# Optimization experiments

Measured on AMD Instinct MI355X. Metric: run time of the kernel, lower is better.

Reference implementation:

```python
import jax, jax.numpy as jnp
import numpy as np

B, N, S, K = 8, 16384, 1024, 32
C_STEM, C_PATCH, PE_DIM = 64, 128, 24
RADIUS = 0.2
NUM_BANDS = PE_DIM // 6  # 4 freq bands, sin+cos per xyz axis -> 3*2*4 = 24


def setup_inputs() -> dict:
    key = jax.random.key(0)
    ks = jax.random.split(key, 6)
    xyz = jax.random.uniform(ks[0], (B, N, 3), dtype=jnp.float32)
    point_feature = jax.random.normal(ks[1], (B, N, C_STEM), dtype=jnp.float32)
    patch_center = jax.random.uniform(ks[2], (B, S, 3), dtype=jnp.float32)
    in_dim = C_STEM + 3 + PE_DIM  # grouped_feature + relative_xyz + pos-enc
    w1 = jax.random.normal(ks[3], (in_dim, C_PATCH), dtype=jnp.float32) / np.sqrt(in_dim)
    b1 = jnp.zeros((C_PATCH,), dtype=jnp.float32)
    w2 = jax.random.normal(ks[4], (C_PATCH, C_PATCH), dtype=jnp.float32) / np.sqrt(C_PATCH)
    b2 = jnp.zeros((C_PATCH,), dtype=jnp.float32)
    return dict(xyz=xyz, point_feature=point_feature, patch_center=patch_center,
                w1=w1, b1=b1, w2=w2, b2=b2)


def query_ball_point(radius, nsample, xyz, new_xyz):
    # Standard PointNet++ ball query. xyz:[B,N,3], new_xyz:[B,S,3] -> idx:[B,S,K]
    n = xyz.shape[1]
    sqrdists = jnp.sum((new_xyz[:, :, None, :] - xyz[:, None, :, :]) ** 2, axis=-1)  # [B,S,N]
    gi = jnp.where(sqrdists > radius * radius, n,
                   jnp.arange(n, dtype=jnp.int32)[None, None, :])
    gi = jnp.sort(gi, axis=-1)[:, :, :nsample]           # first K in-ball indices
    first = gi[:, :, :1]
    gi = jnp.where(gi == n, first, gi)                   # pad misses with first hit
    return jnp.minimum(gi, n - 1)


def index_points(points, idx):
    # points:[B,N,C], idx:[B,S,K] -> [B,S,K,C]
    b = points.shape[0]
    return points[jnp.arange(b)[:, None, None], idx]


def pos_encode(rel):
    # NeRF-style sinusoidal encoding of relative xyz: [...,3] -> [...,PE_DIM]
    freqs = (2.0 ** jnp.arange(NUM_BANDS, dtype=jnp.float32)) * jnp.pi
    ang = rel[..., None] * freqs                          # [...,3,NB]
    enc = jnp.concatenate([jnp.sin(ang), jnp.cos(ang)], axis=-1)  # [...,3,2NB]
    return enc.reshape(rel.shape[:-1] + (PE_DIM,))


def reference(xyz, point_feature, patch_center, w1, b1, w2, b2):
    neighbor_idx = query_ball_point(RADIUS, K, xyz, patch_center)   # [B,S,K]
    grouped_xyz = index_points(xyz, neighbor_idx)                    # [B,S,K,3]
    grouped_feature = index_points(point_feature, neighbor_idx)      # [B,S,K,C_STEM]
    relative_xyz = grouped_xyz - patch_center[:, :, None, :]
    relative_position = pos_encode(relative_xyz)                     # [B,S,K,PE_DIM]
    grouped_input = jnp.concatenate(
        (grouped_feature, relative_xyz, relative_position), axis=-1)  # [B,S,K,91]
    h = jax.nn.relu(grouped_input @ w1 + b1)   # PointMLP 1 (shared per-point MLP)
    h = h @ w2 + b2                            # PointMLP 2 (no activation)
    patch_feature = jnp.max(h, axis=2)         # max-pool over K neighbors -> [B,S,C_PATCH]
    return (patch_feature, neighbor_idx)
```

## Files before the change

kernel.cpp:

```cpp
#include <hip/hip_runtime.h>
#include <hip/hip_bf16.h>

#define B_ 8
#define N_ 16384
#define S_ 1024
#define K_ 32
#define CSTEM 64
#define CPATCH 128
#define INDIM 91
#define LDA 104
#define LDH 136
#define NQ 4

typedef __attribute__((ext_vector_type(8))) short short8v;
typedef __attribute__((ext_vector_type(4))) float f32x4;

static __device__ __forceinline__ unsigned short f2bf(float f) {
  union { float f; unsigned int u; } v; v.f = f;
  return (unsigned short)((v.u + 0x7FFFu + ((v.u >> 16) & 1u)) >> 16);
}

__global__ __launch_bounds__(256) void pack_weights(
    const float* __restrict__ w1, const float* __restrict__ w2,
    unsigned short* __restrict__ w1p, unsigned short* __restrict__ w2p)
{
  const int id = blockIdx.x * 256 + threadIdx.x;
  if (id < 3 * 8 * 64) {
    const int l = id & 63, ct = (id >> 6) & 7, ks = id >> 9;
    const int col = 16 * ct + (l & 15);
    const int kb = 32 * ks + (l >> 4) * 8;
    unsigned short v[8];
    #pragma unroll
    for (int j = 0; j < 8; ++j) {
      const int k = kb + j;
      v[j] = (k < INDIM) ? f2bf(w1[k * CPATCH + col]) : (unsigned short)0;
    }
    *(short8v*)&w1p[(size_t)id * 8] = *(const short8v*)v;
  } else if (id < 3 * 8 * 64 + 4 * 8 * 64) {
    const int id2 = id - 3 * 8 * 64;
    const int l = id2 & 63, ct = (id2 >> 6) & 7, ks = id2 >> 9;
    const int col = 16 * ct + (l & 15);
    const int kb = 32 * ks + (l >> 4) * 8;
    unsigned short v[8];
    #pragma unroll
    for (int j = 0; j < 8; ++j) v[j] = f2bf(w2[(kb + j) * CPATCH + col]);
    *(short8v*)&w2p[(size_t)id2 * 8] = *(const short8v*)v;
  }
}

#define FCOMP(V, IDX) (((IDX) & 3) == 0 ? (V)[(IDX) >> 2].x : \
                       ((IDX) & 3) == 1 ? (V)[(IDX) >> 2].y : \
                       ((IDX) & 3) == 2 ? (V)[(IDX) >> 2].z : (V)[(IDX) >> 2].w)

__global__ __launch_bounds__(256) void fused_patch(
    const float* __restrict__ xyz, const float* __restrict__ pf,
    const float* __restrict__ pc,
    const unsigned short* __restrict__ w1p, const float* __restrict__ b1,
    const unsigned short* __restrict__ w2p, const float* __restrict__ b2,
    float* __restrict__ idx_out, float* __restrict__ out)
{
  const int tid  = threadIdx.x;
  const int lane = tid & 63;
  const int w    = tid >> 6;
  const int bs0  = blockIdx.x * NQ;
  const int b    = bs0 >> 10;

  __shared__ float scen[3 * NQ];
  __shared__ int   sidx[NQ][K_];
  __shared__ float sxyz[NQ][K_][3];
  __shared__ int   sfound[NQ];
  __shared__ __align__(16) unsigned short As[NQ * K_][LDA];
  __shared__ __align__(16) unsigned short Hs[K_][LDH];

  const float* __restrict__ xb  = xyz + (size_t)b * N_ * 3;
  const float* __restrict__ pfb = pf  + (size_t)b * N_ * CSTEM;

  if (tid < 3 * NQ) scen[tid] = pc[bs0 * 3 + tid];
  __syncthreads();

  {
    const int q = w;
    const float cx = scen[q * 3 + 0];
    const float cy = scen[q * 3 + 1];
    const float cz = scen[q * 3 + 2];
    const double rr = 0.2 * 0.2;

    int found = 0;
    for (int base = 0; base < N_; base += 1024) {
      const int i0 = base + lane * 16;
      float4 v[12];
      #pragma unroll
      for (int t = 0; t < 12; ++t)
        v[t] = *(const float4*)&xb[i0 * 3 + t * 4];

      unsigned mask = 0u;
      #pragma unroll
      for (int p = 0; p < 16; ++p) {
        const float X = FCOMP(v, 3 * p + 0);
        const float Y = FCOMP(v, 3 * p + 1);
        const float Z = FCOMP(v, 3 * p + 2);
        const float dxf = X - cx, dyf = Y - cy, dzf = Z - cz;
        const float d2f = fmaf(dxf, dxf, fmaf(dyf, dyf, dzf * dzf));
        bool in;
        if (fabsf(d2f - 0.04f) <= 1e-5f) {
          const double dx = (double)X - (double)cx;
          const double dy = (double)Y - (double)cy;
          const double dz = (double)Z - (double)cz;
          in = (dx * dx + dy * dy + dz * dz) <= rr;
        } else {
          in = (d2f < 0.04f);
        }
        if (in) mask |= (1u << p);
      }

      const int cnt = __popc(mask);
      int incl = cnt;
      #pragma unroll
      for (int d = 1; d < 64; d <<= 1) {
        const int t = __shfl_up(incl, d);
        if (lane >= d) incl += t;
      }
      const int tot = __shfl(incl, 63);

      int pos = found + (incl - cnt);
      #pragma unroll
      for (int p = 0; p < 16; ++p) {
        if (mask & (1u << p)) {
          if (pos < K_) {
            sidx[q][pos] = i0 + p;
            sxyz[q][pos][0] = FCOMP(v, 3 * p + 0);
            sxyz[q][pos][1] = FCOMP(v, 3 * p + 1);
            sxyz[q][pos][2] = FCOMP(v, 3 * p + 2);
          }
          ++pos;
        }
      }
      found += tot;
      if (found >= K_) break;
    }
    if (lane == 0) sfound[q] = found;
  }
  __syncthreads();

  if (tid < NQ && sfound[tid] == 0) {
    sidx[tid][0] = N_ - 1;
    sxyz[tid][0][0] = xb[(N_ - 1) * 3 + 0];
    sxyz[tid][0][1] = xb[(N_ - 1) * 3 + 1];
    sxyz[tid][0][2] = xb[(N_ - 1) * 3 + 2];
  }
  __syncthreads();
  if (tid < NQ * K_) {
    const int q = tid >> 5, j = tid & 31;
    const int fq = sfound[q];
    const int v   = (j < fq && fq > 0) ? sidx[q][j]    : sidx[q][0];
    const float x = (j < fq && fq > 0) ? sxyz[q][j][0] : sxyz[q][0][0];
    const float y = (j < fq && fq > 0) ? sxyz[q][j][1] : sxyz[q][0][1];
    const float z = (j < fq && fq > 0) ? sxyz[q][j][2] : sxyz[q][0][2];
    sidx[q][j] = v;
    sxyz[q][j][0] = x; sxyz[q][j][1] = y; sxyz[q][j][2] = z;
    idx_out[(size_t)bs0 * K_ + tid] = (float)v;
  }
  __syncthreads();

  short8v w1f[3][2], w2f[4][2];
  #pragma unroll
  for (int ks = 0; ks < 3; ++ks)
    #pragma unroll
    for (int t = 0; t < 2; ++t)
      w1f[ks][t] = *(const short8v*)&w1p[((size_t)(ks * 8 + 2 * w + t) * 64 + lane) * 8];
  #pragma unroll
  for (int ks = 0; ks < 4; ++ks)
    #pragma unroll
    for (int t = 0; t < 2; ++t)
      w2f[ks][t] = *(const short8v*)&w2p[((size_t)(ks * 8 + 2 * w + t) * 64 + lane) * 8];
  const float bias1[2] = { b1[32 * w + (lane & 15)], b1[32 * w + 16 + (lane & 15)] };
  const float bias2[2] = { b2[32 * w + (lane & 15)], b2[32 * w + 16 + (lane & 15)] };

  {
    const int row = tid >> 3, sub = tid & 7;
    #pragma unroll
    for (int q = 0; q < NQ; ++q) {
      const int r = sidx[q][row];
      const float4 f0 = *(const float4*)&pfb[(size_t)r * CSTEM + sub * 8];
      const float4 f1 = *(const float4*)&pfb[(size_t)r * CSTEM + sub * 8 + 4];
      unsigned short vv[8];
      vv[0] = f2bf(f0.x); vv[1] = f2bf(f0.y); vv[2] = f2bf(f0.z); vv[3] = f2bf(f0.w);
      vv[4] = f2bf(f1.x); vv[5] = f2bf(f1.y); vv[6] = f2bf(f1.z); vv[7] = f2bf(f1.w);
      *(short8v*)&As[q * K_ + row][sub * 8] = *(const short8v*)vv;
    }
  }
  {
    const int row = tid & 31, j = tid >> 5;
    #pragma unroll
    for (int q = 0; q < NQ; ++q) {
      const float r0 = sxyz[q][row][0] - scen[q * 3 + 0];
      const float r1 = sxyz[q][row][1] - scen[q * 3 + 1];
      const float r2 = sxyz[q][row][2] - scen[q * 3 + 2];
      #pragma unroll
      for (int cc = 0; cc < 4; ++cc) {
        const int c = 64 + 4 * j + cc;
        float val;
        if (c < 67) val = (c == 64) ? r0 : ((c == 65) ? r1 : r2);
        else if (c < 91) {
          const int qq = c - 67, d = qq >> 3, rbit = qq & 7, band = rbit & 3;
          const float rel = (d == 0) ? r0 : ((d == 1) ? r1 : r2);
          const float ang = rel * ((float)(1 << band) * 3.14159265358979323846f);
          val = (rbit < 4) ? __sinf(ang) : __cosf(ang);
        } else val = 0.f;
        As[q * K_ + row][c] = f2bf(val);
      }
    }
  }
  __syncthreads();

  #pragma unroll 1
  for (int q = 0; q < NQ; ++q) {
    f32x4 acc[2][2] = {};
    #pragma unroll
    for (int ks = 0; ks < 3; ++ks) {
      const int k0 = ks * 32 + (lane >> 4) * 8;
      const short8v a0 = *(const short8v*)&As[q * K_ + (lane & 15)][k0];
      const short8v a1 = *(const short8v*)&As[q * K_ + 16 + (lane & 15)][k0];
      acc[0][0] = __builtin_amdgcn_mfma_f32_16x16x32_bf16(a0, w1f[ks][0], acc[0][0], 0, 0, 0);
      acc[0][1] = __builtin_amdgcn_mfma_f32_16x16x32_bf16(a0, w1f[ks][1], acc[0][1], 0, 0, 0);
      acc[1][0] = __builtin_amdgcn_mfma_f32_16x16x32_bf16(a1, w1f[ks][0], acc[1][0], 0, 0, 0);
      acc[1][1] = __builtin_amdgcn_mfma_f32_16x16x32_bf16(a1, w1f[ks][1], acc[1][1], 0, 0, 0);
    }
    #pragma unroll
    for (int rt = 0; rt < 2; ++rt)
      #pragma unroll
      for (int t = 0; t < 2; ++t)
        #pragma unroll
        for (int reg = 0; reg < 4; ++reg) {
          const float h = fmaxf(acc[rt][t][reg] + bias1[t], 0.f);
          const int row = 16 * rt + (lane >> 4) * 4 + reg;
          const int col = 32 * w + 16 * t + (lane & 15);
          Hs[row][col] = f2bf(h);
        }
    __syncthreads();

    f32x4 acc2[2][2] = {};
    #pragma unroll
    for (int ks = 0; ks < 4; ++ks) {
      const int k0 = ks * 32 + (lane >> 4) * 8;
      const short8v a0 = *(const short8v*)&Hs[(lane & 15)][k0];
      const short8v a1 = *(const short8v*)&Hs[16 + (lane & 15)][k0];
      acc2[0][0] = __builtin_amdgcn_mfma_f32_16x16x32_bf16(a0, w2f[ks][0], acc2[0][0], 0, 0, 0);
      acc2[0][1] = __builtin_amdgcn_mfma_f32_16x16x32_bf16(a0, w2f[ks][1], acc2[0][1], 0, 0, 0);
      acc2[1][0] = __builtin_amdgcn_mfma_f32_16x16x32_bf16(a1, w2f[ks][0], acc2[1][0], 0, 0, 0);
      acc2[1][1] = __builtin_amdgcn_mfma_f32_16x16x32_bf16(a1, w2f[ks][1], acc2[1][1], 0, 0, 0);
    }
    float m0 = -3.4e38f, m1 = -3.4e38f;
    #pragma unroll
    for (int rt = 0; rt < 2; ++rt)
      #pragma unroll
      for (int reg = 0; reg < 4; ++reg) {
        m0 = fmaxf(m0, acc2[rt][0][reg]);
        m1 = fmaxf(m1, acc2[rt][1][reg]);
      }
    m0 += bias2[0];
    m1 += bias2[1];
    m0 = fmaxf(m0, __shfl_xor(m0, 16));
    m0 = fmaxf(m0, __shfl_xor(m0, 32));
    m1 = fmaxf(m1, __shfl_xor(m1, 16));
    m1 = fmaxf(m1, __shfl_xor(m1, 32));
    if (lane < 16) {
      out[(size_t)(bs0 + q) * CPATCH + 32 * w + lane]      = m0;
      out[(size_t)(bs0 + q) * CPATCH + 32 * w + 16 + lane] = m1;
    }
    __syncthreads();
  }
}

extern "C" void kernel_launch(void* const* d_in, const int* in_sizes, int n_in,
                              void* d_out, int out_size, void* d_ws, size_t ws_size,
                              hipStream_t stream) {
  const float* xyz = (const float*)d_in[0];
  const float* pf  = (const float*)d_in[1];
  const float* pc  = (const float*)d_in[2];
  const float* w1  = (const float*)d_in[3];
  const float* b1  = (const float*)d_in[4];
  const float* w2  = (const float*)d_in[5];
  const float* b2  = (const float*)d_in[6];

  float* out     = (float*)d_out;
  float* idx_out = out + (size_t)B_ * S_ * CPATCH;

  unsigned short* w1p = (unsigned short*)d_ws;
  unsigned short* w2p = w1p + 96 * 128;

  pack_weights<<<14, 256, 0, stream>>>(w1, w2, w1p, w2p);
  fused_patch<<<B_ * S_ / NQ, 256, 0, stream>>>(xyz, pf, pc, w1p, b1, w2p, b2,
                                                idx_out, out);
}
```

Before: 50.22 us.

## Split ball query into separate kernel and halve queries per MLP block

Moves the ball-query search out of the fused kernel into its own kernel, one wave per query, which writes the float indices. The MLP kernel then reads those indices, gathers xyz from global memory and processes 2 queries per block instead of 4. This aims to decouple the divergent, latency-bound search from the MFMA stage so each kernel gets better occupancy and less shared memory. In exchange it adds a kernel launch and a round trip of the indices through global memory. The MLP body (hidden lines) must now handle NQ=2, since the As tile is sized by NQ.

Result: slower. 53.79 us (+7.1%).

```diff
diff --git a/kernel.cpp b/kernel.cpp
--- a/kernel.cpp
+++ b/kernel.cpp
@@ -10,7 +10,7 @@
 #define INDIM 91
 #define LDA 104
 #define LDH 136
-#define NQ 4
+#define NQ 2
 
 typedef __attribute__((ext_vector_type(8))) short short8v;
 typedef __attribute__((ext_vector_type(4))) float f32x4;
@@ -52,12 +52,87 @@
                        ((IDX) & 3) == 1 ? (V)[(IDX) >> 2].y : \
                        ((IDX) & 3) == 2 ? (V)[(IDX) >> 2].z : (V)[(IDX) >> 2].w)
 
-__global__ __launch_bounds__(256) void fused_patch(
+__global__ __launch_bounds__(256) void ball_query_kernel(
+    const float* __restrict__ xyz, const float* __restrict__ pc,
+    float* __restrict__ idx_out)
+{
+  const int lane = threadIdx.x & 63;
+  const int w    = threadIdx.x >> 6;
+  const int bs   = blockIdx.x * 4 + w;
+  const int b    = bs >> 10;
+
+  __shared__ int sidx[4][K_];
+
+  const float* __restrict__ xb = xyz + (size_t)b * N_ * 3;
+  const float cx = pc[bs * 3 + 0];
+  const float cy = pc[bs * 3 + 1];
+  const float cz = pc[bs * 3 + 2];
+  const double rr = 0.2 * 0.2;
+
+  int found = 0;
+  for (int base = 0; base < N_; base += 1024) {
+    const int i0 = base + lane * 16;
+    float4 v[12];
+    #pragma unroll
+    for (int t = 0; t < 12; ++t)
+      v[t] = *(const float4*)&xb[i0 * 3 + t * 4];
+
+    unsigned mask = 0u;
+    #pragma unroll
+    for (int p = 0; p < 16; ++p) {
+      const float X = FCOMP(v, 3 * p + 0);
+      const float Y = FCOMP(v, 3 * p + 1);
+      const float Z = FCOMP(v, 3 * p + 2);
+      const float dxf = X - cx, dyf = Y - cy, dzf = Z - cz;
+      const float d2f = fmaf(dxf, dxf, fmaf(dyf, dyf, dzf * dzf));
+      bool in;
+      if (fabsf(d2f - 0.04f) <= 1e-5f) {
+        const double dx = (double)X - (double)cx;
+        const double dy = (double)Y - (double)cy;
+        const double dz = (double)Z - (double)cz;
+        in = (dx * dx + dy * dy + dz * dz) <= rr;
+      } else {
+        in = (d2f < 0.04f);
+      }
+      if (in) mask |= (1u << p);
+    }
+
+    const int cnt = __popc(mask);
+    int incl = cnt;
+    #pragma unroll
+    for (int d = 1; d < 64; d <<= 1) {
+      const int t = __shfl_up(incl, d);
+      if (lane >= d) incl += t;
+    }
+    const int tot = __shfl(incl, 63);
+
+    int pos = found + (incl - cnt);
+    #pragma unroll
+    for (int p = 0; p < 16; ++p) {
+      if (mask & (1u << p)) {
+        if (pos < K_) sidx[w][pos] = i0 + p;
+        ++pos;
+      }
+    }
+    found += tot;
+    if (found >= K_) break;
+  }
+
+  if (lane == 0 && found == 0) sidx[w][0] = N_ - 1;
+  __threadfence_block();
+  if (lane < K_) {
+    const int fill = sidx[w][0];
+    const int v = (lane < found) ? sidx[w][lane] : fill;
+    idx_out[(size_t)bs * K_ + lane] = (float)v;
+  }
+}
+
+__global__ __launch_bounds__(256) void patch_mlp_mfma(
     const float* __restrict__ xyz, const float* __restrict__ pf,
     const float* __restrict__ pc,
     const unsigned short* __restrict__ w1p, const float* __restrict__ b1,
     const unsigned short* __restrict__ w2p, const float* __restrict__ b2,
-    float* __restrict__ idx_out, float* __restrict__ out)
+    const float* __restrict__ idx_f, float* __restrict__ out)
 {
   const int tid  = threadIdx.x;
   const int lane = tid & 63;
@@ -67,8 +142,6 @@
 
   __shared__ float scen[3 * NQ];
   __shared__ int   sidx[NQ][K_];
-  __shared__ float sxyz[NQ][K_][3];
-  __shared__ int   sfound[NQ];
   __shared__ __align__(16) unsigned short As[NQ * K_][LDA];
   __shared__ __align__(16) unsigned short Hs[K_][LDH];
 
@@ -76,89 +149,9 @@
   const float* __restrict__ pfb = pf  + (size_t)b * N_ * CSTEM;
 
   if (tid < 3 * NQ) scen[tid] = pc[bs0 * 3 + tid];
-  __syncthreads();
-
-  {
-    const int q = w;
-    const float cx = scen[q * 3 + 0];
-    const float cy = scen[q * 3 + 1];
-    const float cz = scen[q * 3 + 2];
-    const double rr = 0.2 * 0.2;
-
-    int found = 0;
-    for (int base = 0; base < N_; base += 1024) {
-      const int i0 = base + lane * 16;
-      float4 v[12];
-      #pragma unroll
-      for (int t = 0; t < 12; ++t)
-        v[t] = *(const float4*)&xb[i0 * 3 + t * 4];
-
-      unsigned mask = 0u;
-      #pragma unroll
-      for (int p = 0; p < 16; ++p) {
-        const float X = FCOMP(v, 3 * p + 0);
-        const float Y = FCOMP(v, 3 * p + 1);
-        const float Z = FCOMP(v, 3 * p + 2);
-        const float dxf = X - cx, dyf = Y - cy, dzf = Z - cz;
-        const float d2f = fmaf(dxf, dxf, fmaf(dyf, dyf, dzf * dzf));
-        bool in;
-        if (fabsf(d2f - 0.04f) <= 1e-5f) {
-          const double dx = (double)X - (double)cx;
-          const double dy = (double)Y - (double)cy;
-          const double dz = (double)Z - (double)cz;
-          in = (dx * dx + dy * dy + dz * dz) <= rr;
-        } else {
-          in = (d2f < 0.04f);
-        }
-        if (in) mask |= (1u << p);
-      }
-
-      const int cnt = __popc(mask);
-      int incl = cnt;
-      #pragma unroll
-      for (int d = 1; d < 64; d <<= 1) {
-        const int t = __shfl_up(incl, d);
-        if (lane >= d) incl += t;
-      }
-      const int tot = __shfl(incl, 63);
-
-      int pos = found + (incl - cnt);
-      #pragma unroll
-      for (int p = 0; p < 16; ++p) {
-        if (mask & (1u << p)) {
-          if (pos < K_) {
-            sidx[q][pos] = i0 + p;
-            sxyz[q][pos][0] = FCOMP(v, 3 * p + 0);
-            sxyz[q][pos][1] = FCOMP(v, 3 * p + 1);
-            sxyz[q][pos][2] = FCOMP(v, 3 * p + 2);
-          }
-          ++pos;
-        }
-      }
-      found += tot;
-      if (found >= K_) break;
-    }
-    if (lane == 0) sfound[q] = found;
-  }
-  __syncthreads();
-
-  if (tid < NQ && sfound[tid] == 0) {
-    sidx[tid][0] = N_ - 1;
-    sxyz[tid][0][0] = xb[(N_ - 1) * 3 + 0];
-    sxyz[tid][0][1] = xb[(N_ - 1) * 3 + 1];
-    sxyz[tid][0][2] = xb[(N_ - 1) * 3 + 2];
-  }
-  __syncthreads();
   if (tid < NQ * K_) {
     const int q = tid >> 5, j = tid & 31;
-    const int fq = sfound[q];
-    const int v   = (j < fq && fq > 0) ? sidx[q][j]    : sidx[q][0];
-    const float x = (j < fq && fq > 0) ? sxyz[q][j][0] : sxyz[q][0][0];
-    const float y = (j < fq && fq > 0) ? sxyz[q][j][1] : sxyz[q][0][1];
-    const float z = (j < fq && fq > 0) ? sxyz[q][j][2] : sxyz[q][0][2];
-    sidx[q][j] = v;
-    sxyz[q][j][0] = x; sxyz[q][j][1] = y; sxyz[q][j][2] = z;
-    idx_out[(size_t)bs0 * K_ + tid] = (float)v;
+    sidx[q][j] = (int)idx_f[(size_t)(bs0 + q) * K_ + j];
   }
   __syncthreads();
 
@@ -193,9 +186,10 @@
     const int row = tid & 31, j = tid >> 5;
     #pragma unroll
     for (int q = 0; q < NQ; ++q) {
-      const float r0 = sxyz[q][row][0] - scen[q * 3 + 0];
-      const float r1 = sxyz[q][row][1] - scen[q * 3 + 1];
-      const float r2 = sxyz[q][row][2] - scen[q * 3 + 2];
+      const int r = sidx[q][row];
+      const float r0 = xb[r * 3 + 0] - scen[q * 3 + 0];
+      const float r1 = xb[r * 3 + 1] - scen[q * 3 + 1];
+      const float r2 = xb[r * 3 + 2] - scen[q * 3 + 2];
       #pragma unroll
       for (int cc = 0; cc < 4; ++cc) {
         const int c = 64 + 4 * j + cc;
@@ -290,6 +284,7 @@
   unsigned short* w2p = w1p + 96 * 128;
 
   pack_weights<<<14, 256, 0, stream>>>(w1, w2, w1p, w2p);
-  fused_patch<<<B_ * S_ / NQ, 256, 0, stream>>>(xyz, pf, pc, w1p, b1, w2p, b2,
-                                                idx_out, out);
-}
+  ball_query_kernel<<<B_ * S_ / 4, 256, 0, stream>>>(xyz, pc, idx_out);
+  patch_mlp_mfma<<<B_ * S_ / NQ, 256, 0, stream>>>(xyz, pf, pc, w1p, b1, w2p, b2,
+                                                   idx_out, out);
+}
```
